# Kernel tuning notes

Measured on AMD Instinct MI355X. Metric: run time of the kernel, lower is better.

## Reference

```python
import jax, jax.numpy as jnp
import numpy as np

B, T, NF, D, H, F, LTXT, V, NL = 256, 24, 12, 256, 8, 512, 128, 30000, 2
LN_EPS = 1e-5

def _make_pe(max_len, d):
    pos = np.arange(max_len)[:, None].astype(np.float32)
    i = np.arange(d)[None, :]
    angle = pos / np.power(10000.0, (2 * (i // 2)).astype(np.float32) / d)
    pe = np.zeros((max_len, d), dtype=np.float32)
    pe[:, 0::2] = np.sin(angle[:, 0::2])
    pe[:, 1::2] = np.cos(angle[:, 1::2])
    return jnp.asarray(pe)

PE = _make_pe(500, D)

def _ln(x, g, b):
    mu = jnp.mean(x, -1, keepdims=True)
    var = jnp.mean((x - mu) ** 2, -1, keepdims=True)
    return (x - mu) / jnp.sqrt(var + LN_EPS) * g + b

def _encoder(x, lengths, in_W, in_b, attn_W, attn_b, ff_W1, ff_b1, ff_W2, ff_b2, ln_g, ln_b):
    # post-LN transformer encoder with length-based padding masks (dropout = eval/identity)
    Bq, S, Dm = x.shape
    dk = Dm // H
    key_mask = jnp.arange(S)[None, :] < lengths[:, None]          # [B,S]
    npad = key_mask[..., None].astype(x.dtype)                    # zero padded positions
    enc = _ln(x @ in_W.T + in_b, ln_g[0], ln_b[0]) + PE[:S]
    for l in range(attn_W.shape[0]):
        q = (enc @ attn_W[l, 0].T + attn_b[l, 0]).reshape(Bq, S, H, dk)
        k = (enc @ attn_W[l, 1].T + attn_b[l, 1]).reshape(Bq, S, H, dk)
        v = (enc @ attn_W[l, 2].T + attn_b[l, 2]).reshape(Bq, S, H, dk)
        scores = jnp.einsum('bqhd,bkhd->bhqk', q, k) / jnp.sqrt(jnp.float32(dk))
        scores = jnp.where(key_mask[:, None, None, :], scores, jnp.float32(-1e9))
        ctx = jnp.einsum('bhqk,bkhd->bqhd', jax.nn.softmax(scores, -1), v).reshape(Bq, S, Dm)
        enc = _ln(ctx @ attn_W[l, 3].T + attn_b[l, 3] + enc, ln_g[1 + 2 * l], ln_b[1 + 2 * l]) * npad
        ff = jax.nn.relu(enc @ ff_W1[l].T + ff_b1[l]) @ ff_W2[l].T + ff_b2[l]
        enc = _ln(ff + enc, ln_g[2 + 2 * l], ln_b[2 + 2 * l]) * npad
    return enc

def _forward(x, h, m, d, x_m, age, gen, dec_w, dec_b, hd_W, hd_b, gru_Wih, gru_Whh, gru_bih, gru_bhh,
             txt_emb, t_in_W, t_in_b, t_attn_W, t_attn_b, t_ff_W1, t_ff_b1, t_ff_W2, t_ff_b2, t_ln_g, t_ln_b,
             f_in_W, f_in_b, f_attn_W, f_attn_b, f_ff_W1, f_ff_b1, f_ff_W2, f_ff_b2, f_ln_g, f_ln_b,
             f_cls, fc1_W, fc1_b, bn_g, bn_b, fc2_W, fc2_b, txts, txt_lengths):
    # GRU-D input decay: 12 independent Linear(1,1) == elementwise affine over feature dim
    x_d = jnp.exp(-jax.nn.relu(d * dec_w + dec_b))                 # [B,T,NF]
    xc = m * x + (1 - m) * x_d * x + (1 - m) * (1 - x_d) * x_m[None, None, :]

    def step(hc, td):
        d_t, x_t, m_t = td                                          # [B,NF] each
        h_d = jnp.exp(-jax.nn.relu(d_t @ hd_W.T + hd_b))            # hidden decay
        hc = h_d * hc
        gi = jnp.concatenate([x_t, m_t], -1) @ gru_Wih.T + gru_bih  # [B,3D]
        gh = hc @ gru_Whh.T + gru_bhh
        ir, iz, inn = jnp.split(gi, 3, -1)
        hr, hz, hn = jnp.split(gh, 3, -1)
        r = jax.nn.sigmoid(ir + hr)
        z = jax.nn.sigmoid(iz + hz)
        n = jnp.tanh(inn + r * hn)
        hc = (1 - z) * n + z * hc
        return hc, hc

    _, emb = jax.lax.scan(step, h, (d.transpose(1, 0, 2), xc.transpose(1, 0, 2), m.transpose(1, 0, 2)))
    emb = emb.transpose(1, 0, 2)                                    # [B,T,D]

    txt_x = txt_emb[txts]                                           # [B,LTXT,D]
    txt_out = _encoder(txt_x, txt_lengths, t_in_W, t_in_b, t_attn_W, t_attn_b,
                       t_ff_W1, t_ff_b1, t_ff_W2, t_ff_b2, t_ln_g, t_ln_b)

    cls_tok = jnp.broadcast_to(f_cls, (emb.shape[0], 1, D))
    seq = jnp.concatenate([cls_tok, emb, txt_out], 1)               # [B,1+T+LTXT,D]
    fin_len = txt_lengths + emb.shape[1] + 1
    fin = _encoder(seq, fin_len, f_in_W, f_in_b, f_attn_W, f_attn_b,
                   f_ff_W1, f_ff_b1, f_ff_W2, f_ff_b2, f_ln_g, f_ln_b)
    cls = fin[:, 0]
    ci = jnp.concatenate([cls, age[:, None], gen[:, None]], 1)      # [B,D+2]
    h1 = jnp.einsum('bd,khd->kbh', ci, fc1_W) + fc1_b[:, None, :]   # 12 task heads
    h1 = (h1 / jnp.sqrt(1.0 + LN_EPS)) * bn_g[:, None, :] + bn_b[:, None, :]  # BatchNorm1d eval (mean 0, var 1)
    h1 = jax.nn.relu(h1)
    out = jnp.einsum('kbh,koh->kbo', h1, fc2_W) + fc2_b[:, None, :]
    return jax.nn.sigmoid(out)                                      # [12,B,1]

def setup_inputs() -> dict:
    key = jax.random.key(0)
    ks = iter(jax.random.split(key, 64))
    def n(shape, s=0.02):
        return jax.random.normal(next(ks), shape, jnp.float32) * s
    inp = {}
    inp['x'] = jax.random.normal(next(ks), (B, T, NF), jnp.float32)
    inp['h'] = jnp.zeros((B, D), jnp.float32)
    inp['m'] = (jax.random.uniform(next(ks), (B, T, NF)) < 0.7).astype(jnp.float32)
    inp['d'] = jax.random.uniform(next(ks), (B, T, NF)) * 5.0
    inp['x_m'] = jax.random.normal(next(ks), (NF,), jnp.float32)
    inp['age'] = jax.random.uniform(next(ks), (B,))
    inp['gen'] = (jax.random.uniform(next(ks), (B,)) < 0.5).astype(jnp.float32)
    inp['input_lengths'] = jnp.full((B,), T, jnp.int32)
    inp['txts'] = jax.random.randint(next(ks), (B, LTXT), 0, V, jnp.int32)
    inp['txt_lengths'] = jax.random.randint(next(ks), (B,), 64, LTXT + 1, jnp.int32)
    inp['dec_w'] = n((NF,), 0.5); inp['dec_b'] = jnp.zeros((NF,), jnp.float32)
    inp['hd_W'] = n((D, NF), 0.1); inp['hd_b'] = jnp.zeros((D,), jnp.float32)
    inp['gru_Wih'] = n((3 * D, 2 * NF), 0.05); inp['gru_Whh'] = n((3 * D, D), 0.05)
    inp['gru_bih'] = jnp.zeros((3 * D,), jnp.float32); inp['gru_bhh'] = jnp.zeros((3 * D,), jnp.float32)
    inp['txt_emb'] = n((V, D), 0.02)
    for p in ('t_', 'f_'):
        inp[p + 'in_W'] = n((D, D)); inp[p + 'in_b'] = jnp.zeros((D,), jnp.float32)
        inp[p + 'attn_W'] = n((NL, 4, D, D)); inp[p + 'attn_b'] = jnp.zeros((NL, 4, D), jnp.float32)
        inp[p + 'ff_W1'] = n((NL, F, D)); inp[p + 'ff_b1'] = jnp.zeros((NL, F), jnp.float32)
        inp[p + 'ff_W2'] = n((NL, D, F)); inp[p + 'ff_b2'] = jnp.zeros((NL, D), jnp.float32)
        inp[p + 'ln_g'] = jnp.ones((1 + 2 * NL, D), jnp.float32)
        inp[p + 'ln_b'] = jnp.zeros((1 + 2 * NL, D), jnp.float32)
    inp['f_cls'] = n((1, 1, D), 1.0)
    inp['fc1_W'] = n((12, 64, D + 2), 0.05); inp['fc1_b'] = jnp.zeros((12, 64), jnp.float32)
    inp['bn_g'] = jnp.ones((12, 64), jnp.float32); inp['bn_b'] = jnp.zeros((12, 64), jnp.float32)
    inp['fc2_W'] = n((12, 1, 64), 0.1); inp['fc2_b'] = jnp.zeros((12, 1), jnp.float32)
    return inp

def reference(x, h, m, d, x_m, age, gen, input_lengths, txts, txt_lengths,
              dec_w, dec_b, hd_W, hd_b, gru_Wih, gru_Whh, gru_bih, gru_bhh, txt_emb,
              t_in_W, t_in_b, t_attn_W, t_attn_b, t_ff_W1, t_ff_b1, t_ff_W2, t_ff_b2, t_ln_g, t_ln_b,
              f_in_W, f_in_b, f_attn_W, f_attn_b, f_ff_W1, f_ff_b1, f_ff_W2, f_ff_b2, f_ln_g, f_ln_b,
              f_cls, fc1_W, fc1_b, bn_g, bn_b, fc2_W, fc2_b):
    return _forward(x, h, m, d, x_m, age, gen, dec_w, dec_b, hd_W, hd_b, gru_Wih, gru_Whh, gru_bih, gru_bhh,
                    txt_emb, t_in_W, t_in_b, t_attn_W, t_attn_b, t_ff_W1, t_ff_b1, t_ff_W2, t_ff_b2, t_ln_g, t_ln_b,
                    f_in_W, f_in_b, f_attn_W, f_attn_b, f_ff_W1, f_ff_b1, f_ff_W2, f_ff_b2, f_ln_g, f_ln_b,
                    f_cls, fc1_W, fc1_b, bn_g, bn_b, fc2_W, fc2_b, txts, txt_lengths)
```

## Files before the change

### kernel.cpp

```cpp
#include <hip/hip_runtime.h>
#include <cstdio>
#include <cstddef>

#define BB    256
#define TT    24
#define NFEAT 12
#define DIM   256
#define NH    8
#define DKH   32
#define FFD   512
#define SEQ_T 128
#define SEQ_F 153
#define NLAY  2

typedef unsigned short u16;
typedef u16   __attribute__((ext_vector_type(8))) u16x8;
typedef short __attribute__((ext_vector_type(8))) s16x8;
typedef float __attribute__((ext_vector_type(4))) f32x4;

__device__ inline u16 f2bf(float f) {
    union { float f; unsigned u; } v; v.f = f;
    unsigned r = v.u + 0x7FFFu + ((v.u >> 16) & 1u);
    return (u16)(r >> 16);
}
__device__ inline float bf2f(u16 h) {
    union { unsigned u; float f; } v; v.u = ((unsigned)h) << 16;
    return v.f;
}

__device__ __forceinline__ void gload16(const u16* g, u16* l) {
    __builtin_amdgcn_global_load_lds(
        (const __attribute__((address_space(1))) unsigned int*)g,
        (__attribute__((address_space(3))) unsigned int*)l, 16, 0, 0);
}

#define PER_ENC_CAST 1114112
__global__ __launch_bounds__(256) void prep_kernel(
    const float* __restrict__ t_in_W, const float* __restrict__ t_attn_W,
    const float* __restrict__ t_ff_W1, const float* __restrict__ t_ff_W2,
    const float* __restrict__ f_in_W, const float* __restrict__ f_attn_W,
    const float* __restrict__ f_ff_W1, const float* __restrict__ f_ff_W2,
    u16* __restrict__ wbf, float* __restrict__ pe,
    const float* __restrict__ Whh, u16* __restrict__ whhT2)
{
    int blk = blockIdx.x;
    if (blk < 2176) {
        int i = (blk * 256 + threadIdx.x) * 4;
        int e = i >= PER_ENC_CAST;
        int off = i - e * PER_ENC_CAST;
        const float* src;
        if (off < 65536)       { src = (e ? f_in_W   : t_in_W)   + off; }
        else if (off < 589824) { src = (e ? f_attn_W : t_attn_W) + off - 65536; }
        else if (off < 851968) { src = (e ? f_ff_W1  : t_ff_W1)  + off - 589824; }
        else                   { src = (e ? f_ff_W2  : t_ff_W2)  + off - 851968; }
        float4 v = *(const float4*)src;
        ushort4 o;
        o.x = f2bf(v.x); o.y = f2bf(v.y); o.z = f2bf(v.z); o.w = f2bf(v.w);
        *(ushort4*)&wbf[i] = o;
    } else if (blk < 2329) {
        int s = blk - 2176, i = threadIdx.x;
        float e = (float)(2 * (i / 2)) * (1.0f / 256.0f);
        float freq = expf(-e * 9.210340371976184f);
        float ang = (float)s * freq;
        pe[s * 256 + i] = (i & 1) ? cosf(ang) : sinf(ang);
    } else {
        int n = blk - 2329, k = threadIdx.x;
        whhT2[(size_t)(k >> 1) * 1536 + n * 2 + (k & 1)] = f2bf(Whh[(size_t)n * 256 + k]);
    }
}

__global__ __launch_bounds__(768) void grud_kernel(
    const float* __restrict__ x, const float* __restrict__ h0,
    const float* __restrict__ m, const float* __restrict__ dd,
    const float* __restrict__ x_m,
    const float* __restrict__ dec_w, const float* __restrict__ dec_b,
    const float* __restrict__ hd_W, const float* __restrict__ hd_b,
    const float* __restrict__ Wih, const float* __restrict__ bih,
    const u16* __restrict__ WhhT2, const float* __restrict__ bhh,
    float* __restrict__ emb)
{
    int b = blockIdx.x;
    int tid = threadIdx.x;
    int gate = tid >> 8;
    int j = tid & 255;
    __shared__ float hcs[256], hdecs[256], r_s[256], z_s[256];
    __shared__ float dts[12], xcm[24];

    float wih[24];
#pragma unroll
    for (int i = 0; i < 24; i++) wih[i] = Wih[(size_t)tid * 24 + i];
    float bi_ = bih[tid], bh_ = bhh[tid];

    float hdw[12]; float hdb = 0.0f;
    if (tid < 256) {
#pragma unroll
        for (int i = 0; i < 12; i++) hdw[i] = hd_W[tid * 12 + i];
        hdb = hd_b[tid];
        hcs[tid] = h0[(size_t)b * 256 + tid];
    }
    __syncthreads();

    const u16* wcol = WhhT2 + tid * 2;
    for (int t = 0; t < TT; t++) {
        if (tid < 12) {
            size_t idx = ((size_t)b * TT + t) * NFEAT + tid;
            float dv = dd[idx], xv = x[idx], mv = m[idx];
            float xd = expf(-fmaxf(dv * dec_w[tid] + dec_b[tid], 0.0f));
            dts[tid] = dv;
            xcm[tid] = mv * xv + (1.0f - mv) * xd * xv + (1.0f - mv) * (1.0f - xd) * x_m[tid];
            xcm[12 + tid] = mv;
        }
        __syncthreads();
        if (tid < 256) {
            float acc = hdb;
#pragma unroll
            for (int i = 0; i < 12; i++) acc += hdw[i] * dts[i];
            hdecs[tid] = expf(-fmaxf(acc, 0.0f)) * hcs[tid];
        }
        __syncthreads();
        float acc_i = bi_;
#pragma unroll
        for (int i = 0; i < 24; i++) acc_i += wih[i] * xcm[i];
        float a0 = bh_, a1 = 0.0f;
#pragma unroll 8
        for (int k2 = 0; k2 < 128; k2++) {
            unsigned pair = *(const unsigned*)(wcol + (size_t)k2 * 1536);
            a0 = fmaf(bf2f((u16)(pair & 0xFFFFu)), hdecs[2 * k2],     a0);
            a1 = fmaf(bf2f((u16)(pair >> 16)),     hdecs[2 * k2 + 1], a1);
        }
        float acc_h = a0 + a1;
        if (gate == 0) r_s[j] = 1.0f / (1.0f + expf(-(acc_i + acc_h)));
        else if (gate == 1) z_s[j] = 1.0f / (1.0f + expf(-(acc_i + acc_h)));
        __syncthreads();
        if (gate == 2) {
            float n = tanhf(acc_i + r_s[j] * acc_h);
            float hnew = (1.0f - z_s[j]) * n + z_s[j] * hdecs[j];
            hcs[j] = hnew;
            emb[((size_t)b * TT + t) * 256 + j] = hnew;
        }
        __syncthreads();
    }
}

__global__ void gather_kernel(const int* __restrict__ txts, const float* __restrict__ txt_emb,
                              u16* __restrict__ outp) {
    int r = blockIdx.x, i = threadIdx.x;
    outp[(size_t)r * 256 + i] = f2bf(txt_emb[(size_t)txts[r] * 256 + i]);
}

__global__ void build_seq_kernel(const float* __restrict__ emb, const u16* __restrict__ encTb,
                                 const float* __restrict__ fcls, u16* __restrict__ seq) {
    int r = blockIdx.x, i = threadIdx.x;
    int b = r / SEQ_F, s = r - b * SEQ_F;
    u16 v;
    if (s == 0)       v = f2bf(fcls[i]);
    else if (s < 25)  v = f2bf(emb[((size_t)b * TT + (s - 1)) * 256 + i]);
    else              v = encTb[((size_t)b * SEQ_T + (s - 25)) * 256 + i];
    seq[(size_t)r * 256 + i] = v;
}

template <int RELU>
__global__ __launch_bounds__(512) void gemm_wide_kernel(
    const u16* __restrict__ A, const u16* __restrict__ W,
    const float* __restrict__ bias, u16* __restrict__ Cout,
    int M, int N, int K)
{
    __shared__ u16 As[2][128 * 32];
    __shared__ u16 Bs[2][256 * 32];
    const int bm = blockIdx.y * 128, bn = blockIdx.x * 256;
    const int tid = threadIdx.x;
    const int w = tid >> 6, lane = tid & 63;
    const int wm = (w >> 2) * 64, wn = (w & 3) * 64;
    const int l15 = lane & 15, l16 = lane >> 4;
    const int srow = lane >> 2, scol = (lane & 3) * 8;
    f32x4 acc[4][4] = {};

    const u16* ga0 = A + (size_t)(bm + 16 * w + srow) * K + scol;
    const u16* gb0 = W + (size_t)(bn + 16 * w + srow) * K + scol;
    const u16* gb1 = W + (size_t)(bn + 128 + 16 * w + srow) * K + scol;

#define STAGE_W(buf, kk)                                      \
    do {                                                      \
        gload16(ga0 + (kk), &As[buf][16 * w * 32]);           \
        gload16(gb0 + (kk), &Bs[buf][16 * w * 32]);           \
        gload16(gb1 + (kk), &Bs[buf][(128 + 16 * w) * 32]);   \
    } while (0)

    STAGE_W(0, 0);
    __syncthreads();
    int cur = 0;
    for (int k0 = 0; k0 < K; k0 += 32) {
        if (k0 + 32 < K) STAGE_W(cur ^ 1, k0 + 32);
        s16x8 af[4], bfr[4];
#pragma unroll
        for (int i = 0; i < 4; i++)
            af[i] = *(const s16x8*)&As[cur][(wm + i * 16 + l15) * 32 + l16 * 8];
#pragma unroll
        for (int i = 0; i < 4; i++)
            bfr[i] = *(const s16x8*)&Bs[cur][(wn + i * 16 + l15) * 32 + l16 * 8];
#pragma unroll
        for (int mi = 0; mi < 4; mi++)
#pragma unroll
            for (int ni = 0; ni < 4; ni++)
                acc[mi][ni] = __builtin_amdgcn_mfma_f32_16x16x32_bf16(af[mi], bfr[ni], acc[mi][ni], 0, 0, 0);
        __syncthreads();
        cur ^= 1;
    }
#undef STAGE_W
#pragma unroll
    for (int mi = 0; mi < 4; mi++)
#pragma unroll
        for (int ni = 0; ni < 4; ni++) {
            int col = bn + wn + ni * 16 + l15;
            float bv = bias[col];
#pragma unroll
            for (int r = 0; r < 4; r++) {
                int row = bm + wm + mi * 16 + l16 * 4 + r;
                float v = acc[mi][ni][r] + bv;
                if (RELU) v = fmaxf(v, 0.0f);
                Cout[(size_t)row * N + col] = f2bf(v);
            }
        }
}

template <int ADDLN>
__global__ __launch_bounds__(512) void gemm_ln_kernel(
    const u16* __restrict__ A, const u16* __restrict__ W,
    const float* __restrict__ bias, const u16* __restrict__ res,
    const float* __restrict__ pe,
    const float* __restrict__ g, const float* __restrict__ b2,
    const int* __restrict__ lengths, int len_add, int S,
    u16* __restrict__ encbf, int M, int K)
{
    __shared__ u16 As[2][128 * 32];
    __shared__ u16 Bs[2][256 * 32];
    __shared__ float2 red[4][128];
    __shared__ float2 red2[128];
    const int bm = blockIdx.x * 128;
    const int tid = threadIdx.x;
    const int w = tid >> 6, lane = tid & 63;
    const int wm = (w >> 2) * 64, wc = w & 3, wn = wc * 64;
    const int l15 = lane & 15, l16 = lane >> 4;
    const int srow = lane >> 2, scol = (lane & 3) * 8;
    f32x4 acc[4][4] = {};

    const u16* ga0 = A + (size_t)(bm + 16 * w + srow) * K + scol;
    const u16* gb0 = W + (size_t)(16 * w + srow) * K + scol;
    const u16* gb1 = W + (size_t)(128 + 16 * w + srow) * K + scol;

#define STAGE_L(buf, kk)                                      \
    do {                                                      \
        gload16(ga0 + (kk), &As[buf][16 * w * 32]);           \
        gload16(gb0 + (kk), &Bs[buf][16 * w * 32]);           \
        gload16(gb1 + (kk), &Bs[buf][(128 + 16 * w) * 32]);   \
    } while (0)

    STAGE_L(0, 0);
    __syncthreads();
    int cur = 0;
    for (int k0 = 0; k0 < K; k0 += 32) {
        if (k0 + 32 < K) STAGE_L(cur ^ 1, k0 + 32);
        s16x8 af[4], bfr[4];
#pragma unroll
        for (int i = 0; i < 4; i++)
            af[i] = *(const s16x8*)&As[cur][(wm + i * 16 + l15) * 32 + l16 * 8];
#pragma unroll
        for (int i = 0; i < 4; i++)
            bfr[i] = *(const s16x8*)&Bs[cur][(wn + i * 16 + l15) * 32 + l16 * 8];
#pragma unroll
        for (int mi = 0; mi < 4; mi++)
#pragma unroll
            for (int ni = 0; ni < 4; ni++)
                acc[mi][ni] = __builtin_amdgcn_mfma_f32_16x16x32_bf16(af[mi], bfr[ni], acc[mi][ni], 0, 0, 0);
        __syncthreads();
        cur ^= 1;
    }
#undef STAGE_L

    float bcol[4];
#pragma unroll
    for (int ni = 0; ni < 4; ni++) bcol[ni] = bias[wn + ni * 16 + l15];
#pragma unroll
    for (int mi = 0; mi < 4; mi++)
#pragma unroll
        for (int ni = 0; ni < 4; ni++)
#pragma unroll
            for (int r = 0; r < 4; r++) {
                float v = acc[mi][ni][r] + bcol[ni];
                if (ADDLN)
                    v += bf2f(res[(size_t)(bm + wm + mi * 16 + l16 * 4 + r) * 256 + wn + ni * 16 + l15]);
                acc[mi][ni][r] = v;
            }
#pragma unroll
    for (int mi = 0; mi < 4; mi++)
#pragma unroll
        for (int r = 0; r < 4; r++) {
            float s = 0.0f, q = 0.0f;
#pragma unroll
            for (int ni = 0; ni < 4; ni++) { float v = acc[mi][ni][r]; s += v; q += v * v; }
#pragma unroll
            for (int off = 1; off <= 8; off <<= 1) {
                s += __shfl_xor(s, off, 64);
                q += __shfl_xor(q, off, 64);
            }
            if (l15 == 0) {
                float2 p; p.x = s; p.y = q;
                red[wc][wm + mi * 16 + l16 * 4 + r] = p;
            }
        }
    __syncthreads();
    if (tid < 128) {
        float s = 0.0f, q = 0.0f;
#pragma unroll
        for (int c = 0; c < 4; c++) { float2 p = red[c][tid]; s += p.x; q += p.y; }
        float mean = s * (1.0f / 256.0f);
        float var = q * (1.0f / 256.0f) - mean * mean;
        float2 o; o.x = mean; o.y = rsqrtf(var + 1e-5f);
        red2[tid] = o;
    }
    __syncthreads();
#pragma unroll
    for (int mi = 0; mi < 4; mi++)
#pragma unroll
        for (int r = 0; r < 4; r++) {
            int lrow = wm + mi * 16 + l16 * 4 + r;
            int grow = bm + lrow;
            float2 mr = red2[lrow];
            int bb = grow / S, sr = grow - bb * S;
            float mask = 1.0f;
            if (ADDLN) mask = (sr < lengths[bb] + len_add) ? 1.0f : 0.0f;
#pragma unroll
            for (int ni = 0; ni < 4; ni++) {
                int col = wn + ni * 16 + l15;
                float o = (acc[mi][ni][r] - mr.x) * mr.y * g[col] + b2[col];
                if (ADDLN) o *= mask;
                else       o += pe[sr * 256 + col];
                encbf[(size_t)grow * 256 + col] = f2bf(o);
            }
        }
}

__global__ __launch_bounds__(256) void attn_mfma_kernel(
    const u16* __restrict__ qkv, u16* __restrict__ ctx,
    const int* __restrict__ lengths, int len_add, int S)
{
    __shared__ u16 K_lds[160][40];
    __shared__ u16 Vt_lds[32][176];
    __shared__ u16 P_lds[4][16][48];

    const int bh = blockIdx.x;
    const int b = bh >> 3, h = bh & 7;
    const int len = lengths[b] + len_add;
    const int tid = threadIdx.x;
    const int w = tid >> 6;
    const int lane = tid & 63;
    const int l15 = lane & 15, l16 = lane >> 4;

    const u16* kbase = qkv + ((size_t)b * S) * 768 + 256 + h * 32;
    const u16* vbase = kbase + 256;
    for (int chunk = tid; chunk < 160 * 4; chunk += 256) {
        int s = chunk >> 2, d8 = (chunk & 3) * 8;
        u16x8 kv = {}; u16x8 vv = {};
        if (s < S) {
            kv = *(const u16x8*)(kbase + (size_t)s * 768 + d8);
            vv = *(const u16x8*)(vbase + (size_t)s * 768 + d8);
        }
        *(u16x8*)&K_lds[s][d8] = kv;
#pragma unroll
        for (int j = 0; j < 8; j++) Vt_lds[d8 + j][s] = vv[j];
    }
    __syncthreads();

    const f32x4 zero4 = {0.0f, 0.0f, 0.0f, 0.0f};
    const float SCALE = 0.17677669529663687f;

    for (int q0 = w * 16; q0 < S; q0 += 64) {
        const int qr = min(q0 + l15, S - 1);
        s16x8 qf = *(const s16x8*)(qkv + ((size_t)(b * S + qr)) * 768 + h * 32 + l16 * 8);
        f32x4 o0 = zero4, o1 = zero4;
        float mreg = -1e30f, lreg = 0.0f;

        for (int k0 = 0; k0 < len; k0 += 32) {
            s16x8 kf0 = *(const s16x8*)&K_lds[k0 + l15][l16 * 8];
            s16x8 kf1 = *(const s16x8*)&K_lds[k0 + 16 + l15][l16 * 8];
            f32x4 c0 = __builtin_amdgcn_mfma_f32_16x16x32_bf16(kf0, qf, zero4, 0, 0, 0);
            f32x4 c1 = __builtin_amdgcn_mfma_f32_16x16x32_bf16(kf1, qf, zero4, 0, 0, 0);
            float sc[8];
#pragma unroll
            for (int r = 0; r < 4; r++) {
                int key0 = k0 + l16 * 4 + r;
                sc[r]     = (key0 < len)      ? c0[r] * SCALE : -1e30f;
                sc[4 + r] = (key0 + 16 < len) ? c1[r] * SCALE : -1e30f;
            }
            float tmax = sc[0];
#pragma unroll
            for (int i = 1; i < 8; i++) tmax = fmaxf(tmax, sc[i]);
            tmax = fmaxf(tmax, __shfl_xor(tmax, 16, 64));
            tmax = fmaxf(tmax, __shfl_xor(tmax, 32, 64));
            float mnew = fmaxf(mreg, tmax);
            float rescale = expf(mreg - mnew);
            float psum = 0.0f;
            u16 pb[8];
#pragma unroll
            for (int i = 0; i < 8; i++) {
                float p = expf(sc[i] - mnew);
                psum += p;
                pb[i] = f2bf(p);
            }
            psum += __shfl_xor(psum, 16, 64);
            psum += __shfl_xor(psum, 32, 64);
            lreg = lreg * rescale + psum;
            mreg = mnew;
#pragma unroll
            for (int i = 0; i < 4; i++) { o0[i] *= rescale; o1[i] *= rescale; }
#pragma unroll
            for (int r = 0; r < 4; r++) {
                P_lds[w][l15][l16 * 4 + r]      = pb[r];
                P_lds[w][l15][16 + l16 * 4 + r] = pb[4 + r];
            }
            s16x8 pf  = *(const s16x8*)&P_lds[w][l15][l16 * 8];
            s16x8 vf0 = *(const s16x8*)&Vt_lds[l15][k0 + l16 * 8];
            s16x8 vf1 = *(const s16x8*)&Vt_lds[16 + l15][k0 + l16 * 8];
            o0 = __builtin_amdgcn_mfma_f32_16x16x32_bf16(vf0, pf, o0, 0, 0, 0);
            o1 = __builtin_amdgcn_mfma_f32_16x16x32_bf16(vf1, pf, o1, 0, 0, 0);
        }

        float inv = 1.0f / lreg;
        int qg = q0 + l15;
        if (qg < S) {
            size_t ob = ((size_t)(b * S + qg)) * 256 + h * 32;
#pragma unroll
            for (int r = 0; r < 4; r++) {
                ctx[ob + l16 * 4 + r]      = f2bf(o0[r] * inv);
                ctx[ob + 16 + l16 * 4 + r] = f2bf(o1[r] * inv);
            }
        }
    }
}

__global__ __launch_bounds__(64) void classifier_kernel(
    const u16* __restrict__ encFb, const float* __restrict__ age, const float* __restrict__ gen,
    const float* __restrict__ fc1_W, const float* __restrict__ fc1_b,
    const float* __restrict__ bn_g, const float* __restrict__ bn_b,
    const float* __restrict__ fc2_W, const float* __restrict__ fc2_b,
    float* __restrict__ outp)
{
    int k = blockIdx.x, b = blockIdx.y, t = threadIdx.x;
    const u16* cls = encFb + (size_t)b * SEQ_F * 256;
    const float* wrow = fc1_W + ((size_t)k * 64 + t) * 258;
    float acc = fc1_b[k * 64 + t];
    for (int d2 = 0; d2 < 256; d2++) acc += bf2f(cls[d2]) * wrow[d2];
    acc += age[b] * wrow[256] + gen[b] * wrow[257];
    const float RSQ = 0.99999500003749980e0f;
    acc = acc * RSQ * bn_g[k * 64 + t] + bn_b[k * 64 + t];
    acc = fmaxf(acc, 0.0f);
    float p = acc * fc2_W[k * 64 + t];
#pragma unroll
    for (int o = 32; o >= 1; o >>= 1) p += __shfl_xor(p, o, 64);
    if (t == 0) outp[k * 256 + b] = 1.0f / (1.0f + expf(-(p + fc2_b[k])));
}

struct WB { const u16 *inW, *attnW, *ff1W, *ff2W; };

static void run_encoder(u16* enc_bf,
                        u16* actx_b, u16* scr_b,
                        const WB& wb, const float* pe, int S,
                        const float* in_b, const float* attn_b,
                        const float* ff_b1, const float* ff_b2,
                        const float* ln_g, const float* ln_b,
                        const int* lengths, int len_add, hipStream_t stream)
{
    int M = BB * S;
    int MB = M / 128;
    dim3 g512(512 / 256, MB), g768(768 / 256, MB);
    gemm_ln_kernel<0><<<MB, 512, 0, stream>>>(actx_b, wb.inW, in_b, nullptr, pe,
                                              ln_g, ln_b, lengths, len_add, S,
                                              enc_bf, M, 256);
    for (int l = 0; l < NLAY; l++) {
        const u16* wqkv = wb.attnW + (size_t)l * 4 * 65536;
        const u16* wout = wb.attnW + ((size_t)l * 4 + 3) * 65536;
        const float* bqkv = attn_b + (size_t)l * 4 * 256;
        const float* bout = attn_b + ((size_t)l * 4 + 3) * 256;
        gemm_wide_kernel<0><<<g768, 512, 0, stream>>>(enc_bf, wqkv, bqkv, scr_b, M, 768, 256);
        attn_mfma_kernel<<<BB * NH, 256, 0, stream>>>(scr_b, actx_b, lengths, len_add, S);
        gemm_ln_kernel<1><<<MB, 512, 0, stream>>>(actx_b, wout, bout, enc_bf, nullptr,
                                                  ln_g + (1 + 2 * l) * 256, ln_b + (1 + 2 * l) * 256,
                                                  lengths, len_add, S, enc_bf, M, 256);
        gemm_wide_kernel<1><<<g512, 512, 0, stream>>>(enc_bf, wb.ff1W + (size_t)l * 512 * 256,
                                                      ff_b1 + l * 512, scr_b, M, 512, 256);
        gemm_ln_kernel<1><<<MB, 512, 0, stream>>>(scr_b, wb.ff2W + (size_t)l * 256 * 512,
                                                  ff_b2 + l * 256, enc_bf, nullptr,
                                                  ln_g + (2 + 2 * l) * 256, ln_b + (2 + 2 * l) * 256,
                                                  lengths, len_add, S, enc_bf, M, 512);
    }
}

extern "C" void kernel_launch(void* const* d_in, const int* in_sizes, int n_in,
                              void* d_out, int out_size, void* d_ws, size_t ws_size,
                              hipStream_t stream)
{
    const float* x        = (const float*)d_in[0];
    const float* h0       = (const float*)d_in[1];
    const float* m        = (const float*)d_in[2];
    const float* dd       = (const float*)d_in[3];
    const float* x_m      = (const float*)d_in[4];
    const float* age      = (const float*)d_in[5];
    const float* gen      = (const float*)d_in[6];
    const int*   txts     = (const int*)d_in[8];
    const int*   txt_len  = (const int*)d_in[9];
    const float* dec_w    = (const float*)d_in[10];
    const float* dec_b    = (const float*)d_in[11];
    const float* hd_W     = (const float*)d_in[12];
    const float* hd_b     = (const float*)d_in[13];
    const float* gru_Wih  = (const float*)d_in[14];
    const float* gru_Whh  = (const float*)d_in[15];
    const float* gru_bih  = (const float*)d_in[16];
    const float* gru_bhh  = (const float*)d_in[17];
    const float* txt_emb  = (const float*)d_in[18];
    const float* t_in_W   = (const float*)d_in[19];
    const float* t_in_b   = (const float*)d_in[20];
    const float* t_attn_W = (const float*)d_in[21];
    const float* t_attn_b = (const float*)d_in[22];
    const float* t_ff_W1  = (const float*)d_in[23];
    const float* t_ff_b1  = (const float*)d_in[24];
    const float* t_ff_W2  = (const float*)d_in[25];
    const float* t_ff_b2  = (const float*)d_in[26];
    const float* t_ln_g   = (const float*)d_in[27];
    const float* t_ln_b   = (const float*)d_in[28];
    const float* f_in_W   = (const float*)d_in[29];
    const float* f_in_b   = (const float*)d_in[30];
    const float* f_attn_W = (const float*)d_in[31];
    const float* f_attn_b = (const float*)d_in[32];
    const float* f_ff_W1  = (const float*)d_in[33];
    const float* f_ff_b1  = (const float*)d_in[34];
    const float* f_ff_W2  = (const float*)d_in[35];
    const float* f_ff_b2  = (const float*)d_in[36];
    const float* f_ln_g   = (const float*)d_in[37];
    const float* f_ln_b   = (const float*)d_in[38];
    const float* f_cls    = (const float*)d_in[39];
    const float* fc1_W    = (const float*)d_in[40];
    const float* fc1_b    = (const float*)d_in[41];
    const float* bn_g     = (const float*)d_in[42];
    const float* bn_b     = (const float*)d_in[43];
    const float* fc2_W    = (const float*)d_in[44];
    const float* fc2_b    = (const float*)d_in[45];
    float* outp = (float*)d_out;

    const size_t O_PE    = 0;
    const size_t O_WHHT  = 40960;
    const size_t O_EMB   = 237568;
    const size_t O_ENCT  = 1810432;
    const size_t O_ENCF  = 10199040;
    const size_t O_SCR   = 20226048;
    const size_t O_ACTX  = 35266560;
    const size_t O_WBF   = 50307072;
    const size_t TOTALF  = 51421184;

    if (ws_size < TOTALF * sizeof(float)) {
        fprintf(stderr, "kernel_launch: ws_size %zu < required %zu bytes\n",
                ws_size, TOTALF * sizeof(float));
        return;
    }
    float* ws    = (float*)d_ws;
    float* pe    = ws + O_PE;
    u16*   whhT2 = (u16*)(ws + O_WHHT);
    float* emb   = ws + O_EMB;
    u16*   encTb = (u16*)(ws + O_ENCT);
    u16*   encFb = (u16*)(ws + O_ENCF);
    u16*   scr_b = (u16*)(ws + O_SCR);
    u16*   actx_b= (u16*)(ws + O_ACTX);
    u16*   wbf   = (u16*)(ws + O_WBF);

    const size_t PER_ENC = PER_ENC_CAST;
    WB wbT = { wbf + 0,       wbf + 65536,           wbf + 589824,           wbf + 851968 };
    WB wbF = { wbf + PER_ENC, wbf + PER_ENC + 65536, wbf + PER_ENC + 589824, wbf + PER_ENC + 851968 };

    prep_kernel<<<3097, 256, 0, stream>>>(t_in_W, t_attn_W, t_ff_W1, t_ff_W2,
                                          f_in_W, f_attn_W, f_ff_W1, f_ff_W2,
                                          wbf, pe, gru_Whh, whhT2);

    grud_kernel<<<BB, 768, 0, stream>>>(x, h0, m, dd, x_m, dec_w, dec_b, hd_W, hd_b,
                                        gru_Wih, gru_bih, whhT2, gru_bhh, emb);

    gather_kernel<<<BB * SEQ_T, 256, 0, stream>>>(txts, txt_emb, actx_b);
    run_encoder(encTb, actx_b, scr_b, wbT, pe, SEQ_T,
                t_in_b, t_attn_b, t_ff_b1, t_ff_b2, t_ln_g, t_ln_b, txt_len, 0, stream);

    build_seq_kernel<<<BB * SEQ_F, 256, 0, stream>>>(emb, encTb, f_cls, actx_b);
    run_encoder(encFb, actx_b, scr_b, wbF, pe, SEQ_F,
                f_in_b, f_attn_b, f_ff_b1, f_ff_b2, f_ln_g, f_ln_b, txt_len, 25, stream);

    classifier_kernel<<<dim3(12, BB), 64, 0, stream>>>(encFb, age, gen, fc1_W, fc1_b,
                                                       bn_g, bn_b, fc2_W, fc2_b, outp);
}
```

Baseline: 832.6 us.

## Split GRU-D into parallel precompute and MFMA-based batched recurrent scan

Moves the time-independent input projection and hidden decay factors into a separate fully parallel kernel over all batch-time rows. The recurrence becomes a scan kernel that processes 16 batch rows per block and does the hidden-to-hidden matmul with bf16 MFMA, using a fragment-packed Whh layout built in the prep kernel. This replaces the per-batch scalar dot-product loops, which reloaded the full Whh column every step. In exchange only 16 blocks run the serial scan, which leaves most of the GPU idle, and gi/dfac now sit in scratch buffers that are later reused by the encoders.

```diff
diff --git a/kernel.cpp b/kernel.cpp
--- a/kernel.cpp
+++ b/kernel.cpp
@@ -41,7 +41,7 @@
     const float* __restrict__ f_in_W, const float* __restrict__ f_attn_W,
     const float* __restrict__ f_ff_W1, const float* __restrict__ f_ff_W2,
     u16* __restrict__ wbf, float* __restrict__ pe,
-    const float* __restrict__ Whh, u16* __restrict__ whhT2)
+    const float* __restrict__ Whh, u16* __restrict__ wfrag)
 {
     int blk = blockIdx.x;
     if (blk < 2176) {
@@ -65,78 +65,147 @@
         pe[s * 256 + i] = (i & 1) ? cosf(ang) : sinf(ang);
     } else {
         int n = blk - 2329, k = threadIdx.x;
-        whhT2[(size_t)(k >> 1) * 1536 + n * 2 + (k & 1)] = f2bf(Whh[(size_t)n * 256 + k]);
-    }
-}
-
-__global__ __launch_bounds__(768) void grud_kernel(
-    const float* __restrict__ x, const float* __restrict__ h0,
-    const float* __restrict__ m, const float* __restrict__ dd,
-    const float* __restrict__ x_m,
+        int frag = ((k >> 5) * 8 + ((n >> 5) & 7)) * 6 + (n >> 8) * 2 + ((n >> 4) & 1);
+        int off = frag * 512 + (((k >> 3) & 3) * 16 + (n & 15)) * 8 + (k & 7);
+        wfrag[off] = f2bf(Whh[(size_t)n * 256 + k]);
+    }
+}
+
+__global__ __launch_bounds__(256) void grud_pre_kernel(
+    const float* __restrict__ x, const float* __restrict__ m,
+    const float* __restrict__ dd, const float* __restrict__ x_m,
     const float* __restrict__ dec_w, const float* __restrict__ dec_b,
     const float* __restrict__ hd_W, const float* __restrict__ hd_b,
     const float* __restrict__ Wih, const float* __restrict__ bih,
-    const u16* __restrict__ WhhT2, const float* __restrict__ bhh,
-    float* __restrict__ emb)
-{
-    int b = blockIdx.x;
+    float* __restrict__ gi, float* __restrict__ dfac)
+{
+    int rid = blockIdx.x;
     int tid = threadIdx.x;
-    int gate = tid >> 8;
-    int j = tid & 255;
-    __shared__ float hcs[256], hdecs[256], r_s[256], z_s[256];
-    __shared__ float dts[12], xcm[24];
-
-    float wih[24];
-#pragma unroll
-    for (int i = 0; i < 24; i++) wih[i] = Wih[(size_t)tid * 24 + i];
-    float bi_ = bih[tid], bh_ = bhh[tid];
-
-    float hdw[12]; float hdb = 0.0f;
-    if (tid < 256) {
-#pragma unroll
-        for (int i = 0; i < 12; i++) hdw[i] = hd_W[tid * 12 + i];
-        hdb = hd_b[tid];
-        hcs[tid] = h0[(size_t)b * 256 + tid];
+    __shared__ float xcm[24], dts[12];
+    if (tid < 12) {
+        size_t idx = (size_t)rid * 12 + tid;
+        float dv = dd[idx], xv = x[idx], mv = m[idx];
+        float xd = expf(-fmaxf(dv * dec_w[tid] + dec_b[tid], 0.0f));
+        dts[tid] = dv;
+        xcm[tid] = mv * xv + (1.0f - mv) * xd * xv + (1.0f - mv) * (1.0f - xd) * x_m[tid];
+        xcm[12 + tid] = mv;
     }
     __syncthreads();
-
-    const u16* wcol = WhhT2 + tid * 2;
-    for (int t = 0; t < TT; t++) {
-        if (tid < 12) {
-            size_t idx = ((size_t)b * TT + t) * NFEAT + tid;
-            float dv = dd[idx], xv = x[idx], mv = m[idx];
-            float xd = expf(-fmaxf(dv * dec_w[tid] + dec_b[tid], 0.0f));
-            dts[tid] = dv;
-            xcm[tid] = mv * xv + (1.0f - mv) * xd * xv + (1.0f - mv) * (1.0f - xd) * x_m[tid];
-            xcm[12 + tid] = mv;
+#pragma unroll
+    for (int p = 0; p < 3; p++) {
+        int n = p * 256 + tid;
+        const float* wr = Wih + (size_t)n * 24;
+        float a = bih[n];
+#pragma unroll
+        for (int i = 0; i < 24; i++) a += wr[i] * xcm[i];
+        gi[(size_t)rid * 768 + n] = a;
+    }
+    {
+        const float* hw = hd_W + (size_t)tid * 12;
+        float a = hd_b[tid];
+#pragma unroll
+        for (int i = 0; i < 12; i++) a += hw[i] * dts[i];
+        dfac[(size_t)rid * 256 + tid] = expf(-fmaxf(a, 0.0f));
+    }
+}
+
+__global__ __launch_bounds__(512) void grud_scan_kernel(
+    const float* __restrict__ h0, const float* __restrict__ gi,
+    const float* __restrict__ dfac, const u16* __restrict__ wfrag,
+    const float* __restrict__ bhh, float* __restrict__ emb)
+{
+    __shared__ float h_s[16][264];
+    __shared__ float hd_s[16][264];
+    __shared__ u16 hdb_s[16][288];
+    const int b0 = blockIdx.x * 16;
+    const int tid = threadIdx.x;
+    const int w = tid >> 6, lane = tid & 63;
+    const int l15 = lane & 15, l16 = lane >> 4;
+
+    for (int e = tid; e < 4096; e += 512)
+        h_s[e >> 8][e & 255] = h0[(size_t)(b0 + (e >> 8)) * 256 + (e & 255)];
+
+    float bh6[3][2];
+#pragma unroll
+    for (int g = 0; g < 3; g++)
+#pragma unroll
+        for (int jt = 0; jt < 2; jt++)
+            bh6[g][jt] = bhh[g * 256 + w * 32 + jt * 16 + l15];
+    __syncthreads();
+
+    const int hb = tid >> 5, hj = (tid & 31) * 8;
+    const u16* wbase = wfrag + (size_t)lane * 8;
+
+    for (int t = 0; t < 24; t++) {
+        {
+            const float* df = dfac + ((size_t)(b0 + hb) * 24 + t) * 256 + hj;
+            float4 d0 = *(const float4*)df;
+            float4 d1 = *(const float4*)(df + 4);
+            float dv[8] = { d0.x, d0.y, d0.z, d0.w, d1.x, d1.y, d1.z, d1.w };
+            u16 hbv[8];
+#pragma unroll
+            for (int i = 0; i < 8; i++) {
+                float v = h_s[hb][hj + i] * dv[i];
+                hd_s[hb][hj + i] = v;
+                hbv[i] = f2bf(v);
+            }
+            *(u16x8*)&hdb_s[hb][hj] = *(const u16x8*)hbv;
         }
         __syncthreads();
-        if (tid < 256) {
-            float acc = hdb;
-#pragma unroll
-            for (int i = 0; i < 12; i++) acc += hdw[i] * dts[i];
-            hdecs[tid] = expf(-fmaxf(acc, 0.0f)) * hcs[tid];
-        }
-        __syncthreads();
-        float acc_i = bi_;
-#pragma unroll
-        for (int i = 0; i < 24; i++) acc_i += wih[i] * xcm[i];
-        float a0 = bh_, a1 = 0.0f;
-#pragma unroll 8
-        for (int k2 = 0; k2 < 128; k2++) {
-            unsigned pair = *(const unsigned*)(wcol + (size_t)k2 * 1536);
-            a0 = fmaf(bf2f((u16)(pair & 0xFFFFu)), hdecs[2 * k2],     a0);
-            a1 = fmaf(bf2f((u16)(pair >> 16)),     hdecs[2 * k2 + 1], a1);
-        }
-        float acc_h = a0 + a1;
-        if (gate == 0) r_s[j] = 1.0f / (1.0f + expf(-(acc_i + acc_h)));
-        else if (gate == 1) z_s[j] = 1.0f / (1.0f + expf(-(acc_i + acc_h)));
-        __syncthreads();
-        if (gate == 2) {
-            float n = tanhf(acc_i + r_s[j] * acc_h);
-            float hnew = (1.0f - z_s[j]) * n + z_s[j] * hdecs[j];
-            hcs[j] = hnew;
-            emb[((size_t)b * TT + t) * 256 + j] = hnew;
+
+        float giv[3][2][4];
+#pragma unroll
+        for (int g = 0; g < 3; g++)
+#pragma unroll
+            for (int jt = 0; jt < 2; jt++)
+#pragma unroll
+                for (int r = 0; r < 4; r++)
+                    giv[g][jt][r] = gi[((size_t)(b0 + l16 * 4 + r) * 24 + t) * 768
+                                       + g * 256 + w * 32 + jt * 16 + l15];
+
+        f32x4 acc[3][2];
+#pragma unroll
+        for (int g = 0; g < 3; g++)
+#pragma unroll
+            for (int jt = 0; jt < 2; jt++) {
+                f32x4 iv = { bh6[g][jt], bh6[g][jt], bh6[g][jt], bh6[g][jt] };
+                acc[g][jt] = iv;
+            }
+        s16x8 bcur[6], bnxt[6];
+#pragma unroll
+        for (int f = 0; f < 6; f++)
+            bcur[f] = *(const s16x8*)(wbase + (size_t)((0 * 8 + w) * 6 + f) * 512);
+#pragma unroll 1
+        for (int kk = 0; kk < 8; kk++) {
+            if (kk < 7) {
+#pragma unroll
+                for (int f = 0; f < 6; f++)
+                    bnxt[f] = *(const s16x8*)(wbase + (size_t)(((kk + 1) * 8 + w) * 6 + f) * 512);
+            }
+            s16x8 af = *(const s16x8*)&hdb_s[l15][kk * 32 + l16 * 8];
+#pragma unroll
+            for (int g = 0; g < 3; g++)
+#pragma unroll
+                for (int jt = 0; jt < 2; jt++)
+                    acc[g][jt] = __builtin_amdgcn_mfma_f32_16x16x32_bf16(af, bcur[g * 2 + jt], acc[g][jt], 0, 0, 0);
+#pragma unroll
+            for (int f = 0; f < 6; f++) bcur[f] = bnxt[f];
+        }
+
+#pragma unroll
+        for (int jt = 0; jt < 2; jt++) {
+            int j = w * 32 + jt * 16 + l15;
+#pragma unroll
+            for (int r = 0; r < 4; r++) {
+                int b = l16 * 4 + r;
+                float rg = 1.0f / (1.0f + expf(-(giv[0][jt][r] + acc[0][jt][r])));
+                float zg = 1.0f / (1.0f + expf(-(giv[1][jt][r] + acc[1][jt][r])));
+                float ng = tanhf(giv[2][jt][r] + rg * acc[2][jt][r]);
+                float hdv = hd_s[b][j];
+                float hnew = (1.0f - zg) * ng + zg * hdv;
+                h_s[b][j] = hnew;
+                emb[((size_t)(b0 + b) * 24 + t) * 256 + j] = hnew;
+            }
         }
         __syncthreads();
     }
@@ -563,13 +632,15 @@
     }
     float* ws    = (float*)d_ws;
     float* pe    = ws + O_PE;
-    u16*   whhT2 = (u16*)(ws + O_WHHT);
+    u16*   wfrag = (u16*)(ws + O_WHHT);
     float* emb   = ws + O_EMB;
     u16*   encTb = (u16*)(ws + O_ENCT);
     u16*   encFb = (u16*)(ws + O_ENCF);
     u16*   scr_b = (u16*)(ws + O_SCR);
     u16*   actx_b= (u16*)(ws + O_ACTX);
     u16*   wbf   = (u16*)(ws + O_WBF);
+    float* gi    = ws + O_SCR;
+    float* dfac  = ws + O_ACTX;
 
     const size_t PER_ENC = PER_ENC_CAST;
     WB wbT = { wbf + 0,       wbf + 65536,           wbf + 589824,           wbf + 851968 };
@@ -577,10 +648,11 @@
 
     prep_kernel<<<3097, 256, 0, stream>>>(t_in_W, t_attn_W, t_ff_W1, t_ff_W2,
                                           f_in_W, f_attn_W, f_ff_W1, f_ff_W2,
-                                          wbf, pe, gru_Whh, whhT2);
-
-    grud_kernel<<<BB, 768, 0, stream>>>(x, h0, m, dd, x_m, dec_w, dec_b, hd_W, hd_b,
-                                        gru_Wih, gru_bih, whhT2, gru_bhh, emb);
+                                          wbf, pe, gru_Whh, wfrag);
+
+    grud_pre_kernel<<<BB * TT, 256, 0, stream>>>(x, m, dd, x_m, dec_w, dec_b,
+                                                 hd_W, hd_b, gru_Wih, gru_bih, gi, dfac);
+    grud_scan_kernel<<<16, 512, 0, stream>>>(h0, gi, dfac, wfrag, gru_bhh, emb);
 
     gather_kernel<<<BB * SEQ_T, 256, 0, stream>>>(txts, txt_emb, actx_b);
     run_encoder(encTb, actx_b, scr_b, wbT, pe, SEQ_T,
```

New measurement: 883.1 us. 6.1% more time.
